# Kernel optimization log

Hardware: AMD Instinct MI355X
Metric: run time of the kernel (lower is better)

The kernel has to match this reference:

```python
import jax, jax.numpy as jnp
import numpy as np

B, T, V, E, U, OUT = 1024, 64, 30, 128, 512, 20


def _lstm(x, W, Uh, b, reverse=False, return_seq=True):
    """Keras-style LSTM (gate order i,f,g,o). x: [B,T,D]. Returns [B,T,U] or [B,U]."""
    nu = Uh.shape[0]
    if reverse:
        x = x[:, ::-1]
    xz = jnp.einsum('btd,dg->btg', x, W) + b  # [B,T,4U] input projection, precomputed

    def step(carry, z_t):
        h, c = carry
        z = z_t + h @ Uh
        i, f, g, o = jnp.split(z, 4, axis=-1)
        c = jax.nn.sigmoid(f) * c + jax.nn.sigmoid(i) * jnp.tanh(g)
        h = jax.nn.sigmoid(o) * jnp.tanh(c)
        return (h, c), h

    bsz = x.shape[0]
    init = (jnp.zeros((bsz, nu), x.dtype), jnp.zeros((bsz, nu), x.dtype))
    (h_last, _), hs = jax.lax.scan(step, init, jnp.swapaxes(xz, 0, 1))
    if return_seq:
        hs = jnp.swapaxes(hs, 0, 1)  # [B,T,U]
        if reverse:
            hs = hs[:, ::-1]
        return hs
    return h_last


def setup_inputs() -> dict:
    key = jax.random.key(0)
    ks = jax.random.split(key, 14)
    f32 = jnp.float32

    def n(k, shape, s=0.05):
        return jax.random.normal(k, shape, f32) * s

    G = 4 * U
    return {
        'x': jax.random.randint(ks[0], (B, T), 0, V, dtype=jnp.int32),
        'emb': n(ks[1], (V, E)),
        # layer 1 forward / backward directions
        'W1f': n(ks[2], (E, G)), 'U1f': n(ks[3], (U, G)), 'b1f': jnp.zeros((G,), f32),
        'W1b': n(ks[4], (E, G)), 'U1b': n(ks[5], (U, G)), 'b1b': jnp.zeros((G,), f32),
        # layer 2 forward / backward directions (input dim = 2U from concat)
        'W2f': n(ks[6], (2 * U, G)), 'U2f': n(ks[7], (U, G)), 'b2f': jnp.zeros((G,), f32),
        'W2b': n(ks[8], (2 * U, G)), 'U2b': n(ks[9], (U, G)), 'b2b': jnp.zeros((G,), f32),
        # dense head
        'Wd': n(ks[10], (2 * U, 2 * U)), 'bd': jnp.zeros((2 * U,), f32),
        'Wo': n(ks[11], (2 * U, OUT)), 'bo': jnp.zeros((OUT,), f32),
    }


def reference(x, emb, W1f, U1f, b1f, W1b, U1b, b1b,
              W2f, U2f, b2f, W2b, U2b, b2b, Wd, bd, Wo, bo):
    e = emb[x]  # [B,T,E] embedding lookup
    # Bidirectional LSTM 1, return_sequences=True, concat merge -> [B,T,2U]
    h1 = jnp.concatenate([
        _lstm(e, W1f, U1f, b1f),
        _lstm(e, W1b, U1b, b1b, reverse=True),
    ], axis=-1)
    # Bidirectional LSTM 2, return_sequences=False -> [B,2U]
    h2 = jnp.concatenate([
        _lstm(h1, W2f, U2f, b2f, return_seq=False),
        _lstm(h1, W2b, U2b, b2b, reverse=True, return_seq=False),
    ], axis=-1)
    d = jax.nn.relu(h2 @ Wd + bd)  # Dense(2U, relu)
    return d @ Wo + bo             # Dense(output_len), [B,OUT]
```

## Files before the change

### kernel.cpp

```cpp
#include <hip/hip_runtime.h>
#include <hip/hip_bf16.h>

typedef __hip_bfloat16 bf16;
typedef __attribute__((ext_vector_type(4))) float f32x4;
typedef __attribute__((ext_vector_type(8))) short s16x8;

__device__ __forceinline__ float sigf(float x) {
    return 1.0f / (1.0f + __expf(-x));
}
__device__ __forceinline__ float tanh_f(float x) {
    float ax = fabsf(x);
    float e = __expf(-2.0f * ax);
    float r = (1.0f - e) / (1.0f + e);
    return x < 0.0f ? -r : r;
}

#define GLL16(src, ldst)                                                      \
    __builtin_amdgcn_global_load_lds(                                         \
        (const __attribute__((address_space(1))) void*)(src),                 \
        (__attribute__((address_space(3))) void*)(ldst), 16, 0, 0)

__global__ void k_embw(const float* __restrict__ emb,
                       const float* __restrict__ W1f, const float* __restrict__ b1f,
                       const float* __restrict__ W1b, const float* __restrict__ b1b,
                       float* __restrict__ embW) {
    int c = blockIdx.x * 256 + threadIdx.x;
    int v = blockIdx.y;
    int d = blockIdx.z;
    const float* W = d ? W1b : W1f;
    const float* b = d ? b1b : b1f;
    float acc = b[c];
    const float* er = emb + v * 128;
#pragma unroll 8
    for (int e = 0; e < 128; ++e) acc += er[e] * W[e * 2048 + c];
    int n = ((c & 511) << 2) | (c >> 9);
    embW[(d * 30 + v) * 2048 + n] = acc;
}

__global__ void k_b2r(const float* __restrict__ b2f, const float* __restrict__ b2b,
                      float* __restrict__ dst) {
    int i = blockIdx.x * 256 + threadIdx.x;
    int d = i >> 11, n = i & 2047;
    int c = ((n & 3) << 9) | (n >> 2);
    dst[i] = (d ? b2b : b2f)[c];
}

template<int REORDER>
__global__ void k_trans(const float* __restrict__ src, bf16* __restrict__ dst,
                        int ncols, int kpitch, int koff) {
    __shared__ float tile[64][65];
    int k0 = blockIdx.x * 64;
    int c0 = blockIdx.y * 64;
    int tid = threadIdx.x;
#pragma unroll
    for (int i = 0; i < 16; ++i) {
        int seg = tid + i * 256;
        int r = seg >> 6, cc = seg & 63;
        tile[r][cc] = src[(size_t)(k0 + r) * ncols + c0 + cc];
    }
    __syncthreads();
#pragma unroll
    for (int i = 0; i < 16; ++i) {
        int seg = tid + i * 256;
        int nl = seg >> 6, kl = seg & 63;
        int c = c0 + nl;
        int n = REORDER ? (((c & 511) << 2) | (c >> 9)) : c;
        int kabs = koff + k0 + kl;
        dst[(size_t)n * kpitch + (kabs ^ ((n & 7) << 3))] =
            __float2bfloat16(tile[kl][nl]);
    }
}

template<int MODE>
__global__ __launch_bounds__(256, 2)
void k_step(const bf16* __restrict__ A1, const bf16* __restrict__ A2,
            const bf16* __restrict__ Bt, const float* __restrict__ table,
            const int* __restrict__ xin, float* __restrict__ c_st,
            bf16* __restrict__ h_out, bf16* __restrict__ h1s, int t)
{
    constexpr int NCH = (MODE == 0) ? 8 : (MODE == 1) ? 24 : 16;
    constexpr int BP  = (MODE == 0) ? 512 : (MODE == 1) ? 1536 : 1024;

    __shared__ __align__(16) short ldss[32768];

    const int tid  = threadIdx.x;
    const int lane = tid & 63;
    const int wv   = tid >> 6;
    const int wm   = (wv >> 1) << 6;
    const int wn   = (wv & 1) << 6;

    int n0, m0;
    if constexpr (MODE == 2) {
        n0 = (blockIdx.x & 7) << 7;
        m0 = (blockIdx.x >> 3) << 7;
    } else {
        const int xcd = blockIdx.x & 7, y = blockIdx.x >> 3;
        n0 = (((xcd << 1) | (y >> 4))) << 7;
        m0 = (y & 15) << 7;
    }

    const int dir = (MODE == 2) ? 0 : (m0 >= 1024);
    const int t_a = dir ? 63 - t : t;

    const char* a1b;
    if constexpr (MODE == 1)
        a1b = (const char*)(A1 + ((size_t)t_a << 20) + ((size_t)(m0 & 1023) << 10));
    else
        a1b = (const char*)(A1 + (size_t)m0 * 512);
    const char* const btb = (const char*)(Bt + (size_t)dir * 2048 * BP + (size_t)n0 * BP);
    const char* const a2b = (const char*)A2;

    auto stage = [&](int c, int half) {
        char* base = (char*)ldss + half * 32768;
#pragma unroll
        for (int i = 0; i < 4; ++i) {
            const int u = i * 256 + tid;
            const int r = u >> 3, j = u & 7;
            const char* src;
            if constexpr (MODE == 0)
                src = a1b + r * 1024 + c * 128 + j * 16;
            else if constexpr (MODE == 1)
                src = (c < 16) ? a1b + r * 2048 + c * 128 + j * 16
                               : a2b + (size_t)(m0 + r) * 1024 + (c - 16) * 128 + j * 16;
            else
                src = (c < 8) ? a1b + r * 1024 + c * 128 + j * 16
                              : a2b + (size_t)(m0 + r) * 1024 + (c - 8) * 128 + j * 16;
            GLL16(src, base + (i * 256 + wv * 64) * 16);
        }
#pragma unroll
        for (int i = 0; i < 4; ++i) {
            const int u = i * 256 + tid;
            const int r = u >> 3, j = u & 7;
            const char* src = btb + (size_t)r * (BP * 2) + c * 128 + j * 16;
            GLL16(src, base + 16384 + (i * 256 + wv * 64) * 16);
        }
    };

    f32x4 acc[4][4];
#pragma unroll
    for (int i = 0; i < 4; ++i)
#pragma unroll
        for (int j = 0; j < 4; ++j) acc[i][j] = (f32x4){0.f, 0.f, 0.f, 0.f};

    stage(0, 0);

    const int rl = lane & 15;
    const int q8 = (lane >> 4) << 3;
    const int xk = (rl & 7) << 3;

    for (int c = 0; c < NCH; ++c) {
        __syncthreads();
        if (c + 1 < NCH) stage(c + 1, (c + 1) & 1);
        const short* as = ldss + (c & 1) * 16384;
        const short* bs = as + 8192;
#pragma unroll
        for (int ks = 0; ks < 2; ++ks) {
            const int eo = ((ks << 5) + q8) ^ xk;
            s16x8 af[4], bq[4];
#pragma unroll
            for (int f = 0; f < 4; ++f)
                af[f] = *(const s16x8*)&as[(wm + f * 16 + rl) * 64 + eo];
#pragma unroll
            for (int f = 0; f < 4; ++f)
                bq[f] = *(const s16x8*)&bs[(wn + f * 16 + rl) * 64 + eo];
#pragma unroll
            for (int fm = 0; fm < 4; ++fm)
#pragma unroll
                for (int fn = 0; fn < 4; ++fn)
                    acc[fm][fn] = __builtin_amdgcn_mfma_f32_16x16x32_bf16(
                        af[fm], bq[fn], acc[fm][fn], 0, 0, 0);
        }
    }

    if constexpr (MODE == 2) {
#pragma unroll
        for (int fn = 0; fn < 4; ++fn) {
            const int col = n0 + wn + fn * 16 + rl;
            const float bdv = table[col];
#pragma unroll
            for (int fm = 0; fm < 4; ++fm) {
                const int rb = m0 + wm + fm * 16 + ((lane >> 4) << 2);
#pragma unroll
                for (int r = 0; r < 4; ++r) {
                    float v = acc[fm][fn][r] + bdv;
                    h_out[(size_t)(rb + r) * 1024 + col] =
                        __float2bfloat16(v > 0.f ? v : 0.f);
                }
            }
        }
    } else {
        float* z = (float*)ldss;
        const int u0 = n0 >> 2;
        for (int half = 0; half < 2; ++half) {
            __syncthreads();
            if ((wv >> 1) == half) {
#pragma unroll
                for (int fm = 0; fm < 4; ++fm)
#pragma unroll
                    for (int fn = 0; fn < 4; ++fn) {
                        const int zr = fm * 16 + ((lane >> 4) << 2);
                        const int zc = wn + fn * 16 + rl;
#pragma unroll
                        for (int r = 0; r < 4; ++r)
                            z[(zr + r) * 132 + zc] = acc[fm][fn][r];
                    }
            }
            __syncthreads();
#pragma unroll 2
            for (int j = 0; j < 8; ++j) {
                const int cid = j * 256 + tid;
                const int ml = cid >> 5;
                const int ul = cid & 31;
                const int mg = m0 + half * 64 + ml;
                const int b  = mg & 1023;
                float4 z4 = *(float4*)&z[ml * 132 + (ul << 2)];
                const float* tab;
                if constexpr (MODE == 0) {
                    const int v = xin[(b << 6) + t_a];
                    tab = table + (size_t)(dir * 30 + v) * 2048;
                } else {
                    tab = table + dir * 2048;
                }
                const float4 tv = *(const float4*)&tab[n0 + (ul << 2)];
                const float zi = z4.x + tv.x, zf = z4.y + tv.y;
                const float zg = z4.z + tv.z, zo = z4.w + tv.w;
                const float ig = sigf(zi), fg = sigf(zf);
                const float gg = tanh_f(zg), og = sigf(zo);
                const size_t cu = (size_t)mg * 512 + u0 + ul;
                const float cn = fg * c_st[cu] + ig * gg;
                c_st[cu] = cn;
                const float h = og * tanh_f(cn);
                const int us = (u0 + ul) ^ ((mg & 7) << 3);
                h_out[(size_t)mg * 512 + us] = __float2bfloat16(h);
                if constexpr (MODE == 0) {
                    const int col = (((dir << 9) | (u0 + ul)) ^ ((b & 7) << 3));
                    h1s[(((size_t)t_a << 10) + b) * 1024 + col] =
                        __float2bfloat16(h);
                }
            }
        }
    }
}

__global__ __launch_bounds__(256)
void k_out(const bf16* __restrict__ dbuf, const float* __restrict__ Wo,
           const float* __restrict__ bo, float* __restrict__ out) {
    int b = blockIdx.x, tid = threadIdx.x;
    int wv = tid >> 6, lane = tid & 63;
    float acc[5] = {0.f, 0.f, 0.f, 0.f, 0.f};
    for (int kk = 0; kk < 1024; kk += 64) {
        float a = __bfloat162float(dbuf[b * 1024 + kk + lane]);
#pragma unroll
        for (int j = 0; j < 5; ++j)
            acc[j] += a * Wo[(kk + lane) * 20 + wv + j * 4];
    }
#pragma unroll
    for (int j = 0; j < 5; ++j) {
        float s = acc[j];
        for (int off = 32; off; off >>= 1) s += __shfl_down(s, off, 64);
        if (lane == 0) out[b * 20 + wv + j * 4] = s + bo[wv + j * 4];
    }
}

extern "C" void kernel_launch(void* const* d_in, const int* in_sizes, int n_in,
                              void* d_out, int out_size, void* d_ws, size_t ws_size,
                              hipStream_t stream) {
    const int*   x   = (const int*)  d_in[0];
    const float* emb = (const float*)d_in[1];
    const float* W1f = (const float*)d_in[2];
    const float* U1f = (const float*)d_in[3];
    const float* b1f = (const float*)d_in[4];
    const float* W1b = (const float*)d_in[5];
    const float* U1b = (const float*)d_in[6];
    const float* b1b = (const float*)d_in[7];
    const float* W2f = (const float*)d_in[8];
    const float* U2f = (const float*)d_in[9];
    const float* b2f = (const float*)d_in[10];
    const float* W2b = (const float*)d_in[11];
    const float* U2b = (const float*)d_in[12];
    const float* b2b = (const float*)d_in[13];
    const float* Wd  = (const float*)d_in[14];
    const float* bd  = (const float*)d_in[15];
    const float* Wo  = (const float*)d_in[16];
    const float* bo  = (const float*)d_in[17];

    char* ws = (char*)d_ws;
    float* embW = (float*)(ws + 0);
    float* b2r  = (float*)(ws + 491520);
    bf16* Ut1   = (bf16*)(ws + 507904);
    bf16* BigBt = (bf16*)(ws + 4702208);
    bf16* Wdt   = (bf16*)(ws + 17285120);
    bf16* hA    = (bf16*)(ws + 19382272);
    bf16* hB    = (bf16*)(ws + 21479424);
    float* cst  = (float*)(ws + 23576576);
    bf16* dbuf  = (bf16*)(ws + 27770880);
    bf16* h1seq = (bf16*)(ws + 29868032);

    k_embw<<<dim3(8, 30, 2), 256, 0, stream>>>(emb, W1f, b1f, W1b, b1b, embW);
    k_b2r<<<16, 256, 0, stream>>>(b2f, b2b, b2r);
    k_trans<1><<<dim3(8, 32), 256, 0, stream>>>(U1f, Ut1,              2048, 512, 0);
    k_trans<1><<<dim3(8, 32), 256, 0, stream>>>(U1b, Ut1 + 2048 * 512, 2048, 512, 0);
    k_trans<1><<<dim3(16, 32), 256, 0, stream>>>(W2f, BigBt,                2048, 1536, 0);
    k_trans<1><<<dim3(8, 32), 256, 0, stream>>>(U2f, BigBt,                2048, 1536, 1024);
    k_trans<1><<<dim3(16, 32), 256, 0, stream>>>(W2b, BigBt + 2048 * 1536, 2048, 1536, 0);
    k_trans<1><<<dim3(8, 32), 256, 0, stream>>>(U2b, BigBt + 2048 * 1536, 2048, 1536, 1024);
    k_trans<0><<<dim3(16, 16), 256, 0, stream>>>(Wd, Wdt, 1024, 1024, 0);

    hipMemsetAsync(hA, 0, (size_t)2048 * 512 * sizeof(bf16), stream);
    hipMemsetAsync(cst, 0, (size_t)2048 * 512 * sizeof(float), stream);
    bf16 *hin = hA, *hout = hB;
    for (int t = 0; t < 64; ++t) {
        k_step<0><<<256, 256, 0, stream>>>(
            hin, (const bf16*)nullptr, Ut1, embW, x, cst, hout, h1seq, t);
        bf16* tmp = hin; hin = hout; hout = tmp;
    }

    hipMemsetAsync(hin, 0, (size_t)2048 * 512 * sizeof(bf16), stream);
    hipMemsetAsync(cst, 0, (size_t)2048 * 512 * sizeof(float), stream);
    for (int t = 0; t < 64; ++t) {
        k_step<1><<<256, 256, 0, stream>>>(
            h1seq, hin, BigBt, b2r, (const int*)nullptr, cst, hout,
            (bf16*)nullptr, t);
        bf16* tmp = hin; hin = hout; hout = tmp;
    }

    k_step<2><<<64, 256, 0, stream>>>(
        hin, hin + (size_t)1024 * 512, Wdt, bd, (const int*)nullptr,
        (float*)nullptr, dbuf, (bf16*)nullptr, 0);
    k_out<<<1024, 256, 0, stream>>>(dbuf, Wo, bo, (float*)d_out);
}
```

Baseline: 2.603 ms.

## Run each LSTM layer as one persistent cooperative kernel with register-resident recurrent weights

Each layer's 64 per-timestep launches are replaced by a single cooperative kernel that loops over time and uses grid.sync between steps. A non-cooperative per-step fallback is kept. Every block loads its slice of the recurrent weight matrix into registers once, so per-step shared-memory staging of U is dropped, and the tile is reshaped to 128x32 per wave. The aim is to remove launch overhead and repeated weight traffic, at the cost of heavy register pressure (one block per CU), grid-wide barrier latency, and reliance on all 256 blocks being co-resident.

```diff
diff --git a/kernel.cpp b/kernel.cpp
--- a/kernel.cpp
+++ b/kernel.cpp
@@ -1,5 +1,8 @@
 #include <hip/hip_runtime.h>
 #include <hip/hip_bf16.h>
+#include <hip/hip_cooperative_groups.h>
+
+namespace cg = cooperative_groups;
 
 typedef __hip_bfloat16 bf16;
 typedef __attribute__((ext_vector_type(4))) float f32x4;
@@ -45,7 +48,7 @@
     dst[i] = (d ? b2b : b2f)[c];
 }
 
-template<int REORDER>
+template<int REORDER, int XOR>
 __global__ void k_trans(const float* __restrict__ src, bf16* __restrict__ dst,
                         int ncols, int kpitch, int koff) {
     __shared__ float tile[64][65];
@@ -66,144 +69,174 @@
         int c = c0 + nl;
         int n = REORDER ? (((c & 511) << 2) | (c >> 9)) : c;
         int kabs = koff + k0 + kl;
-        dst[(size_t)n * kpitch + (kabs ^ ((n & 7) << 3))] =
-            __float2bfloat16(tile[kl][nl]);
-    }
-}
-
-template<int MODE>
-__global__ __launch_bounds__(256, 2)
-void k_step(const bf16* __restrict__ A1, const bf16* __restrict__ A2,
-            const bf16* __restrict__ Bt, const float* __restrict__ table,
-            const int* __restrict__ xin, float* __restrict__ c_st,
-            bf16* __restrict__ h_out, bf16* __restrict__ h1s, int t)
+        int ks = XOR ? (kabs ^ ((n & 7) << 3)) : kabs;
+        dst[(size_t)n * kpitch + ks] = __float2bfloat16(tile[kl][nl]);
+    }
+}
+
+template<int LAYER>
+__global__ __launch_bounds__(256, 1)
+void l_run(const bf16* __restrict__ Bres, const bf16* __restrict__ W2t,
+           bf16* __restrict__ h1s, const float* __restrict__ table,
+           const int* __restrict__ xin, float* __restrict__ c_st,
+           bf16* __restrict__ h0, bf16* __restrict__ h1, int t0, int t1)
 {
-    constexpr int NCH = (MODE == 0) ? 8 : (MODE == 1) ? 24 : 16;
-    constexpr int BP  = (MODE == 0) ? 512 : (MODE == 1) ? 1536 : 1024;
+    cg::grid_group grid = cg::this_grid();
+    constexpr int NCH = (LAYER == 1) ? 8 : 24;
 
     __shared__ __align__(16) short ldss[32768];
 
     const int tid  = threadIdx.x;
     const int lane = tid & 63;
     const int wv   = tid >> 6;
-    const int wm   = (wv >> 1) << 6;
-    const int wn   = (wv & 1) << 6;
-
-    int n0, m0;
-    if constexpr (MODE == 2) {
-        n0 = (blockIdx.x & 7) << 7;
-        m0 = (blockIdx.x >> 3) << 7;
-    } else {
-        const int xcd = blockIdx.x & 7, y = blockIdx.x >> 3;
-        n0 = (((xcd << 1) | (y >> 4))) << 7;
-        m0 = (y & 15) << 7;
-    }
-
-    const int dir = (MODE == 2) ? 0 : (m0 >= 1024);
-    const int t_a = dir ? 63 - t : t;
-
-    const char* a1b;
-    if constexpr (MODE == 1)
-        a1b = (const char*)(A1 + ((size_t)t_a << 20) + ((size_t)(m0 & 1023) << 10));
-    else
-        a1b = (const char*)(A1 + (size_t)m0 * 512);
-    const char* const btb = (const char*)(Bt + (size_t)dir * 2048 * BP + (size_t)n0 * BP);
-    const char* const a2b = (const char*)A2;
-
-    auto stage = [&](int c, int half) {
-        char* base = (char*)ldss + half * 32768;
-#pragma unroll
-        for (int i = 0; i < 4; ++i) {
-            const int u = i * 256 + tid;
-            const int r = u >> 3, j = u & 7;
-            const char* src;
-            if constexpr (MODE == 0)
-                src = a1b + r * 1024 + c * 128 + j * 16;
-            else if constexpr (MODE == 1)
-                src = (c < 16) ? a1b + r * 2048 + c * 128 + j * 16
-                               : a2b + (size_t)(m0 + r) * 1024 + (c - 16) * 128 + j * 16;
-            else
-                src = (c < 8) ? a1b + r * 1024 + c * 128 + j * 16
-                              : a2b + (size_t)(m0 + r) * 1024 + (c - 8) * 128 + j * 16;
-            GLL16(src, base + (i * 256 + wv * 64) * 16);
-        }
-#pragma unroll
-        for (int i = 0; i < 4; ++i) {
-            const int u = i * 256 + tid;
-            const int r = u >> 3, j = u & 7;
-            const char* src = btb + (size_t)r * (BP * 2) + c * 128 + j * 16;
-            GLL16(src, base + 16384 + (i * 256 + wv * 64) * 16);
-        }
-    };
-
-    f32x4 acc[4][4];
-#pragma unroll
-    for (int i = 0; i < 4; ++i)
-#pragma unroll
-        for (int j = 0; j < 4; ++j) acc[i][j] = (f32x4){0.f, 0.f, 0.f, 0.f};
-
-    stage(0, 0);
-
-    const int rl = lane & 15;
-    const int q8 = (lane >> 4) << 3;
-    const int xk = (rl & 7) << 3;
-
-    for (int c = 0; c < NCH; ++c) {
-        __syncthreads();
-        if (c + 1 < NCH) stage(c + 1, (c + 1) & 1);
-        const short* as = ldss + (c & 1) * 16384;
-        const short* bs = as + 8192;
-#pragma unroll
-        for (int ks = 0; ks < 2; ++ks) {
-            const int eo = ((ks << 5) + q8) ^ xk;
-            s16x8 af[4], bq[4];
-#pragma unroll
-            for (int f = 0; f < 4; ++f)
-                af[f] = *(const s16x8*)&as[(wm + f * 16 + rl) * 64 + eo];
-#pragma unroll
-            for (int f = 0; f < 4; ++f)
-                bq[f] = *(const s16x8*)&bs[(wn + f * 16 + rl) * 64 + eo];
-#pragma unroll
-            for (int fm = 0; fm < 4; ++fm)
-#pragma unroll
-                for (int fn = 0; fn < 4; ++fn)
-                    acc[fm][fn] = __builtin_amdgcn_mfma_f32_16x16x32_bf16(
-                        af[fm], bq[fn], acc[fm][fn], 0, 0, 0);
-        }
-    }
-
-    if constexpr (MODE == 2) {
-#pragma unroll
-        for (int fn = 0; fn < 4; ++fn) {
-            const int col = n0 + wn + fn * 16 + rl;
-            const float bdv = table[col];
-#pragma unroll
-            for (int fm = 0; fm < 4; ++fm) {
-                const int rb = m0 + wm + fm * 16 + ((lane >> 4) << 2);
-#pragma unroll
-                for (int r = 0; r < 4; ++r) {
-                    float v = acc[fm][fn][r] + bdv;
-                    h_out[(size_t)(rb + r) * 1024 + col] =
-                        __float2bfloat16(v > 0.f ? v : 0.f);
-                }
-            }
-        }
-    } else {
+    const int xcd  = blockIdx.x & 7, yy = blockIdx.x >> 3;
+    const int n0   = ((xcd << 1) | (yy >> 4)) << 7;
+    const int m0   = (yy & 15) << 7;
+    const int dir  = (m0 >= 1024);
+    const int rl   = lane & 15;
+    const int q8   = (lane >> 4) << 3;
+    const int xk   = (rl & 7) << 3;
+    const int u0   = n0 >> 2;
+
+    s16x8 bres[2][16];
+    {
+        const bf16* bp = Bres + ((size_t)dir * 2048 + n0 + (wv << 5) + rl) * 512 + q8;
+#pragma unroll
+        for (int fn = 0; fn < 2; ++fn)
+#pragma unroll
+            for (int ks = 0; ks < 16; ++ks)
+                bres[fn][ks] = *(const s16x8*)(bp + fn * (16 * 512) + ks * 32);
+    }
+
+    const char* const btb = (LAYER == 2)
+        ? (const char*)(W2t + ((size_t)dir * 2048 + n0) * 1024) : nullptr;
+
+#pragma unroll 1
+    for (int t = t0; t < t1; ++t) {
+        const bf16* hin  = (t & 1) ? h1 : h0;
+        bf16*       hout = (t & 1) ? h0 : h1;
+        const int t_a = dir ? 63 - t : t;
+        const char* a1b = nullptr;
+        if (LAYER == 2)
+            a1b = (const char*)(h1s + ((size_t)t_a << 20) + ((size_t)(m0 & 1023) << 10));
+        const char* const arb = (const char*)(hin + (size_t)m0 * 512);
+
+        auto stage = [&](int c, int buf) {
+#pragma unroll
+            for (int i = 0; i < 4; ++i) {
+                const int u = i * 256 + tid;
+                const int r = u >> 3, j = u & 7;
+                const char* src;
+                if (LAYER == 1)
+                    src = arb + r * 1024 + c * 128 + j * 16;
+                else
+                    src = (c < 16) ? a1b + r * 2048 + c * 128 + j * 16
+                                   : arb + r * 1024 + (c - 16) * 128 + j * 16;
+                GLL16(src, (char*)ldss + buf * 16384 + (i * 256 + wv * 64) * 16);
+            }
+            if (LAYER == 2 && c < 16) {
+#pragma unroll
+                for (int i = 0; i < 4; ++i) {
+                    const int u = i * 256 + tid;
+                    const int r = u >> 3, j = u & 7;
+                    GLL16(btb + (size_t)r * 2048 + c * 128 + j * 16,
+                          (char*)ldss + 32768 + buf * 16384 + (i * 256 + wv * 64) * 16);
+                }
+            }
+        };
+
+        f32x4 acc[8][2];
+#pragma unroll
+        for (int i = 0; i < 8; ++i) {
+            acc[i][0] = (f32x4){0.f, 0.f, 0.f, 0.f};
+            acc[i][1] = (f32x4){0.f, 0.f, 0.f, 0.f};
+        }
+
+        stage(0, 0);
+
+        if constexpr (LAYER == 2) {
+#pragma unroll 2
+            for (int c = 0; c < 16; ++c) {
+                __syncthreads();
+                stage(c + 1, (c + 1) & 1);
+                const short* as = ldss + (c & 1) * 8192;
+                const short* bs = ldss + 16384 + (c & 1) * 8192;
+#pragma unroll
+                for (int ks = 0; ks < 2; ++ks) {
+                    const int eo = ((ks << 5) + q8) ^ xk;
+                    s16x8 af[8], bq[2];
+#pragma unroll
+                    for (int f = 0; f < 8; ++f)
+                        af[f] = *(const s16x8*)&as[(f * 16 + rl) * 64 + eo];
+#pragma unroll
+                    for (int fn = 0; fn < 2; ++fn)
+                        bq[fn] = *(const s16x8*)&bs[((wv << 5) + fn * 16 + rl) * 64 + eo];
+#pragma unroll
+                    for (int fm = 0; fm < 8; ++fm)
+#pragma unroll
+                        for (int fn = 0; fn < 2; ++fn)
+                            acc[fm][fn] = __builtin_amdgcn_mfma_f32_16x16x32_bf16(
+                                af[fm], bq[fn], acc[fm][fn], 0, 0, 0);
+                }
+            }
+#pragma unroll
+            for (int cc = 0; cc < 8; ++cc) {
+                const int c = 16 + cc;
+                __syncthreads();
+                if (c + 1 < NCH) stage(c + 1, (c + 1) & 1);
+                const short* as = ldss + (c & 1) * 8192;
+#pragma unroll
+                for (int ks = 0; ks < 2; ++ks) {
+                    const int eo = ((ks << 5) + q8) ^ xk;
+                    s16x8 af[8];
+#pragma unroll
+                    for (int f = 0; f < 8; ++f)
+                        af[f] = *(const s16x8*)&as[(f * 16 + rl) * 64 + eo];
+#pragma unroll
+                    for (int fm = 0; fm < 8; ++fm)
+#pragma unroll
+                        for (int fn = 0; fn < 2; ++fn)
+                            acc[fm][fn] = __builtin_amdgcn_mfma_f32_16x16x32_bf16(
+                                af[fm], bres[fn][cc * 2 + ks], acc[fm][fn], 0, 0, 0);
+                }
+            }
+        } else {
+#pragma unroll
+            for (int c = 0; c < 8; ++c) {
+                __syncthreads();
+                if (c + 1 < NCH) stage(c + 1, (c + 1) & 1);
+                const short* as = ldss + (c & 1) * 8192;
+#pragma unroll
+                for (int ks = 0; ks < 2; ++ks) {
+                    const int eo = ((ks << 5) + q8) ^ xk;
+                    s16x8 af[8];
+#pragma unroll
+                    for (int f = 0; f < 8; ++f)
+                        af[f] = *(const s16x8*)&as[(f * 16 + rl) * 64 + eo];
+#pragma unroll
+                    for (int fm = 0; fm < 8; ++fm)
+#pragma unroll
+                        for (int fn = 0; fn < 2; ++fn)
+                            acc[fm][fn] = __builtin_amdgcn_mfma_f32_16x16x32_bf16(
+                                af[fm], bres[fn][c * 2 + ks], acc[fm][fn], 0, 0, 0);
+                }
+            }
+        }
+
         float* z = (float*)ldss;
-        const int u0 = n0 >> 2;
+#pragma unroll
         for (int half = 0; half < 2; ++half) {
             __syncthreads();
-            if ((wv >> 1) == half) {
-#pragma unroll
-                for (int fm = 0; fm < 4; ++fm)
-#pragma unroll
-                    for (int fn = 0; fn < 4; ++fn) {
-                        const int zr = fm * 16 + ((lane >> 4) << 2);
-                        const int zc = wn + fn * 16 + rl;
-#pragma unroll
-                        for (int r = 0; r < 4; ++r)
-                            z[(zr + r) * 132 + zc] = acc[fm][fn][r];
-                    }
+#pragma unroll
+            for (int fm = 0; fm < 4; ++fm) {
+                const int zr = fm * 16 + ((lane >> 4) << 2);
+#pragma unroll
+                for (int fn = 0; fn < 2; ++fn) {
+                    const int zc = (wv << 5) + fn * 16 + rl;
+#pragma unroll
+                    for (int r = 0; r < 4; ++r)
+                        z[(zr + r) * 132 + zc] = acc[half * 4 + fm][fn][r];
+                }
             }
             __syncthreads();
 #pragma unroll 2
@@ -215,7 +248,7 @@
                 const int b  = mg & 1023;
                 float4 z4 = *(float4*)&z[ml * 132 + (ul << 2)];
                 const float* tab;
-                if constexpr (MODE == 0) {
+                if constexpr (LAYER == 1) {
                     const int v = xin[(b << 6) + t_a];
                     tab = table + (size_t)(dir * 30 + v) * 2048;
                 } else {
@@ -231,12 +264,106 @@
                 c_st[cu] = cn;
                 const float h = og * tanh_f(cn);
                 const int us = (u0 + ul) ^ ((mg & 7) << 3);
-                h_out[(size_t)mg * 512 + us] = __float2bfloat16(h);
-                if constexpr (MODE == 0) {
+                hout[(size_t)mg * 512 + us] = __float2bfloat16(h);
+                if constexpr (LAYER == 1) {
                     const int col = (((dir << 9) | (u0 + ul)) ^ ((b & 7) << 3));
                     h1s[(((size_t)t_a << 10) + b) * 1024 + col] =
                         __float2bfloat16(h);
                 }
+            }
+        }
+
+        if (t + 1 < t1) {
+            __threadfence();
+            grid.sync();
+        }
+    }
+}
+
+__global__ __launch_bounds__(256, 2)
+void k_dense(const bf16* __restrict__ hin, const bf16* __restrict__ Bt,
+             const float* __restrict__ bd, bf16* __restrict__ dbuf)
+{
+    __shared__ __align__(16) short ldss[32768];
+    const int tid  = threadIdx.x;
+    const int lane = tid & 63;
+    const int wv   = tid >> 6;
+    const int wm   = (wv >> 1) << 6;
+    const int wn   = (wv & 1) << 6;
+    const int n0   = (blockIdx.x & 7) << 7;
+    const int m0   = (blockIdx.x >> 3) << 7;
+
+    const char* const a1b = (const char*)(hin + (size_t)m0 * 512);
+    const char* const a2b = (const char*)(hin + (size_t)1024 * 512);
+    const char* const btb = (const char*)(Bt + (size_t)n0 * 1024);
+
+    auto stage = [&](int c, int buf) {
+#pragma unroll
+        for (int i = 0; i < 4; ++i) {
+            const int u = i * 256 + tid;
+            const int r = u >> 3, j = u & 7;
+            const char* src = (c < 8)
+                ? a1b + r * 1024 + c * 128 + j * 16
+                : a2b + (size_t)(m0 + r) * 1024 + (c - 8) * 128 + j * 16;
+            GLL16(src, (char*)ldss + buf * 16384 + (i * 256 + wv * 64) * 16);
+        }
+#pragma unroll
+        for (int i = 0; i < 4; ++i) {
+            const int u = i * 256 + tid;
+            const int r = u >> 3, j = u & 7;
+            GLL16(btb + (size_t)r * 2048 + c * 128 + j * 16,
+                  (char*)ldss + 32768 + buf * 16384 + (i * 256 + wv * 64) * 16);
+        }
+    };
+
+    f32x4 acc[4][4];
+#pragma unroll
+    for (int i = 0; i < 4; ++i)
+#pragma unroll
+        for (int j = 0; j < 4; ++j) acc[i][j] = (f32x4){0.f, 0.f, 0.f, 0.f};
+
+    stage(0, 0);
+    const int rl = lane & 15;
+    const int q8 = (lane >> 4) << 3;
+    const int xk = (rl & 7) << 3;
+
+#pragma unroll 2
+    for (int c = 0; c < 16; ++c) {
+        __syncthreads();
+        if (c + 1 < 16) stage(c + 1, (c + 1) & 1);
+        const short* as = ldss + (c & 1) * 8192;
+        const short* bs = ldss + 16384 + (c & 1) * 8192;
+#pragma unroll
+        for (int ks = 0; ks < 2; ++ks) {
+            const int eo = ((ks << 5) + q8) ^ xk;
+            s16x8 af[4], bq[4];
+#pragma unroll
+            for (int f = 0; f < 4; ++f)
+                af[f] = *(const s16x8*)&as[(wm + f * 16 + rl) * 64 + eo];
+#pragma unroll
+            for (int f = 0; f < 4; ++f)
+                bq[f] = *(const s16x8*)&bs[(wn + f * 16 + rl) * 64 + eo];
+#pragma unroll
+            for (int fm = 0; fm < 4; ++fm)
+#pragma unroll
+                for (int fn = 0; fn < 4; ++fn)
+                    acc[fm][fn] = __builtin_amdgcn_mfma_f32_16x16x32_bf16(
+                        af[fm], bq[fn], acc[fm][fn], 0, 0, 0);
+        }
+    }
+
+#pragma unroll
+    for (int fn = 0; fn < 4; ++fn) {
+        const int col = n0 + wn + fn * 16 + rl;
+        const float bdv = bd[col];
+#pragma unroll
+        for (int fm = 0; fm < 4; ++fm) {
+            const int rb = m0 + wm + fm * 16 + ((lane >> 4) << 2);
+#pragma unroll
+            for (int r = 0; r < 4; ++r) {
+                float v = acc[fm][fn][r] + bdv;
+                dbuf[(size_t)(rb + r) * 1024 + col] =
+                    __float2bfloat16(v > 0.f ? v : 0.f);
             }
         }
     }
@@ -288,7 +415,8 @@
     float* embW = (float*)(ws + 0);
     float* b2r  = (float*)(ws + 491520);
     bf16* Ut1   = (bf16*)(ws + 507904);
-    bf16* BigBt = (bf16*)(ws + 4702208);
+    bf16* Ut2   = (bf16*)(ws + 4702208);
+    bf16* W2t   = (bf16*)(ws + 8896512);
     bf16* Wdt   = (bf16*)(ws + 17285120);
     bf16* hA    = (bf16*)(ws + 19382272);
     bf16* hB    = (bf16*)(ws + 21479424);
@@ -298,34 +426,71 @@
 
     k_embw<<<dim3(8, 30, 2), 256, 0, stream>>>(emb, W1f, b1f, W1b, b1b, embW);
     k_b2r<<<16, 256, 0, stream>>>(b2f, b2b, b2r);
-    k_trans<1><<<dim3(8, 32), 256, 0, stream>>>(U1f, Ut1,              2048, 512, 0);
-    k_trans<1><<<dim3(8, 32), 256, 0, stream>>>(U1b, Ut1 + 2048 * 512, 2048, 512, 0);
-    k_trans<1><<<dim3(16, 32), 256, 0, stream>>>(W2f, BigBt,                2048, 1536, 0);
-    k_trans<1><<<dim3(8, 32), 256, 0, stream>>>(U2f, BigBt,                2048, 1536, 1024);
-    k_trans<1><<<dim3(16, 32), 256, 0, stream>>>(W2b, BigBt + 2048 * 1536, 2048, 1536, 0);
-    k_trans<1><<<dim3(8, 32), 256, 0, stream>>>(U2b, BigBt + 2048 * 1536, 2048, 1536, 1024);
-    k_trans<0><<<dim3(16, 16), 256, 0, stream>>>(Wd, Wdt, 1024, 1024, 0);
+    k_trans<1, 0><<<dim3(8, 32), 256, 0, stream>>>(U1f, Ut1,              2048, 512, 0);
+    k_trans<1, 0><<<dim3(8, 32), 256, 0, stream>>>(U1b, Ut1 + 2048 * 512, 2048, 512, 0);
+    k_trans<1, 0><<<dim3(8, 32), 256, 0, stream>>>(U2f, Ut2,              2048, 512, 0);
+    k_trans<1, 0><<<dim3(8, 32), 256, 0, stream>>>(U2b, Ut2 + 2048 * 512, 2048, 512, 0);
+    k_trans<1, 1><<<dim3(16, 32), 256, 0, stream>>>(W2f, W2t,               2048, 1024, 0);
+    k_trans<1, 1><<<dim3(16, 32), 256, 0, stream>>>(W2b, W2t + 2048 * 1024, 2048, 1024, 0);
+    k_trans<0, 1><<<dim3(16, 16), 256, 0, stream>>>(Wd, Wdt, 1024, 1024, 0);
+
+    int dev = 0;
+    hipGetDevice(&dev);
+    int coopAttr = 0, cus = 0;
+    hipDeviceGetAttribute(&coopAttr, hipDeviceAttributeCooperativeLaunch, dev);
+    hipDeviceGetAttribute(&cus, hipDeviceAttributeMultiprocessorCount, dev);
+    int nb1 = 0, nb2 = 0;
+    hipOccupancyMaxActiveBlocksPerMultiprocessor(&nb1, l_run<1>, 256, 0);
+    hipOccupancyMaxActiveBlocksPerMultiprocessor(&nb2, l_run<2>, 256, 0);
+    const bool coop1 = coopAttr && nb1 > 0 && (long)nb1 * cus >= 256;
+    const bool coop2 = coopAttr && nb2 > 0 && (long)nb2 * cus >= 256;
 
     hipMemsetAsync(hA, 0, (size_t)2048 * 512 * sizeof(bf16), stream);
     hipMemsetAsync(cst, 0, (size_t)2048 * 512 * sizeof(float), stream);
-    bf16 *hin = hA, *hout = hB;
-    for (int t = 0; t < 64; ++t) {
-        k_step<0><<<256, 256, 0, stream>>>(
-            hin, (const bf16*)nullptr, Ut1, embW, x, cst, hout, h1seq, t);
-        bf16* tmp = hin; hin = hout; hout = tmp;
-    }
-
-    hipMemsetAsync(hin, 0, (size_t)2048 * 512 * sizeof(bf16), stream);
+    {
+        const bf16* Bres = Ut1;  const bf16* w2 = nullptr;  bf16* h1sp = h1seq;
+        const float* tab = embW; const int* xi = x;         float* cs = cst;
+        bf16* h0p = hA;          bf16* h1p = hB;
+        int t0 = 0, t1 = 64;
+        bool done = false;
+        if (coop1) {
+            void* args[] = {&Bres, &w2, &h1sp, &tab, &xi, &cs, &h0p, &h1p, &t0, &t1};
+            void (*f1)(const bf16*, const bf16*, bf16*, const float*, const int*,
+                       float*, bf16*, bf16*, int, int) = l_run<1>;
+            done = hipLaunchCooperativeKernel(reinterpret_cast<void*>(f1),
+                                              dim3(256), dim3(256), args, 0,
+                                              stream) == hipSuccess;
+        }
+        if (!done)
+            for (int t = 0; t < 64; ++t)
+                l_run<1><<<256, 256, 0, stream>>>(Ut1, (const bf16*)nullptr,
+                                                  h1seq, embW, x, cst, hA, hB,
+                                                  t, t + 1);
+    }
+
+    hipMemsetAsync(hA, 0, (size_t)2048 * 512 * sizeof(bf16), stream);
     hipMemsetAsync(cst, 0, (size_t)2048 * 512 * sizeof(float), stream);
-    for (int t = 0; t < 64; ++t) {
-        k_step<1><<<256, 256, 0, stream>>>(
-            h1seq, hin, BigBt, b2r, (const int*)nullptr, cst, hout,
-            (bf16*)nullptr, t);
-        bf16* tmp = hin; hin = hout; hout = tmp;
-    }
-
-    k_step<2><<<64, 256, 0, stream>>>(
-        hin, hin + (size_t)1024 * 512, Wdt, bd, (const int*)nullptr,
-        (float*)nullptr, dbuf, (bf16*)nullptr, 0);
+    {
+        const bf16* Bres = Ut2;  const bf16* w2 = W2t;  bf16* h1sp = h1seq;
+        const float* tab = b2r;  const int* xi = nullptr;  float* cs = cst;
+        bf16* h0p = hA;          bf16* h1p = hB;
+        int t0 = 0, t1 = 64;
+        bool done = false;
+        if (coop2) {
+            void* args[] = {&Bres, &w2, &h1sp, &tab, &xi, &cs, &h0p, &h1p, &t0, &t1};
+            void (*f2)(const bf16*, const bf16*, bf16*, const float*, const int*,
+                       float*, bf16*, bf16*, int, int) = l_run<2>;
+            done = hipLaunchCooperativeKernel(reinterpret_cast<void*>(f2),
+                                              dim3(256), dim3(256), args, 0,
+                                              stream) == hipSuccess;
+        }
+        if (!done)
+            for (int t = 0; t < 64; ++t)
+                l_run<2><<<256, 256, 0, stream>>>(Ut2, W2t, h1seq, b2r,
+                                                  (const int*)nullptr, cst,
+                                                  hA, hB, t, t + 1);
+    }
+
+    k_dense<<<64, 256, 0, stream>>>(hA, Wdt, bd, dbuf);
     k_out<<<1024, 256, 0, stream>>>(dbuf, Wo, bo, (float*)d_out);
 }
```

Result: slower. 3.275 ms (+25.8%).

## Halve LSTM step tile width to launch 512 blocks and split dense kernel

Applied to the files above, without the earlier changes.

The recurrent step kernel now uses a 128x64 output tile instead of 128x128, so each step launches 512 blocks instead of 256. The aim is to fill more of the GPU's compute units during the latency-bound per-timestep GEMMs. The gate epilogue is rewritten to work on one 128x64 tile in a single pass. The dense head moves into its own kernel that keeps the 128x128 tiling. The cost is that each block reuses the A operand less, so more of the A tile is reloaded across blocks. The new XOR template flag is always set to 1, so it changes nothing yet.

```diff
diff --git a/kernel.cpp b/kernel.cpp
--- a/kernel.cpp
+++ b/kernel.cpp
@@ -45,7 +45,7 @@
     dst[i] = (d ? b2b : b2f)[c];
 }
 
-template<int REORDER>
+template<int REORDER, int XOR>
 __global__ void k_trans(const float* __restrict__ src, bf16* __restrict__ dst,
                         int ncols, int kpitch, int koff) {
     __shared__ float tile[64][65];
@@ -66,8 +66,8 @@
         int c = c0 + nl;
         int n = REORDER ? (((c & 511) << 2) | (c >> 9)) : c;
         int kabs = koff + k0 + kl;
-        dst[(size_t)n * kpitch + (kabs ^ ((n & 7) << 3))] =
-            __float2bfloat16(tile[kl][nl]);
+        int ks = XOR ? (kabs ^ ((n & 7) << 3)) : kabs;
+        dst[(size_t)n * kpitch + ks] = __float2bfloat16(tile[kl][nl]);
     }
 }
 
@@ -78,40 +78,38 @@
             const int* __restrict__ xin, float* __restrict__ c_st,
             bf16* __restrict__ h_out, bf16* __restrict__ h1s, int t)
 {
-    constexpr int NCH = (MODE == 0) ? 8 : (MODE == 1) ? 24 : 16;
-    constexpr int BP  = (MODE == 0) ? 512 : (MODE == 1) ? 1536 : 1024;
-
-    __shared__ __align__(16) short ldss[32768];
+    constexpr int NCH = (MODE == 0) ? 8 : 24;
+    constexpr int BP  = (MODE == 0) ? 512 : 1536;
+
+    __shared__ __align__(16) short ldss[24576];
 
     const int tid  = threadIdx.x;
     const int lane = tid & 63;
     const int wv   = tid >> 6;
-    const int wm   = (wv >> 1) << 6;
-    const int wn   = (wv & 1) << 6;
-
-    int n0, m0;
-    if constexpr (MODE == 2) {
-        n0 = (blockIdx.x & 7) << 7;
-        m0 = (blockIdx.x >> 3) << 7;
-    } else {
-        const int xcd = blockIdx.x & 7, y = blockIdx.x >> 3;
-        n0 = (((xcd << 1) | (y >> 4))) << 7;
-        m0 = (y & 15) << 7;
-    }
-
-    const int dir = (MODE == 2) ? 0 : (m0 >= 1024);
+    const int wm   = wv << 5;
+
+    const int xcd = blockIdx.x & 7, idx = blockIdx.x >> 3;
+    const int n0  = ((xcd << 2) | (idx >> 4)) << 6;
+    const int m0  = (idx & 15) << 7;
+
+    const int dir = (m0 >= 1024);
     const int t_a = dir ? 63 - t : t;
+    const int rl  = lane & 15;
+    const int q8  = (lane >> 4) << 3;
+    const int q4  = (lane >> 4) << 2;
+    const int xk  = (rl & 7) << 3;
+    const int u0  = n0 >> 2;
 
     const char* a1b;
     if constexpr (MODE == 1)
         a1b = (const char*)(A1 + ((size_t)t_a << 20) + ((size_t)(m0 & 1023) << 10));
     else
         a1b = (const char*)(A1 + (size_t)m0 * 512);
-    const char* const btb = (const char*)(Bt + (size_t)dir * 2048 * BP + (size_t)n0 * BP);
+    const char* const btb = (const char*)(Bt + ((size_t)dir * 2048 + n0) * BP);
     const char* const a2b = (const char*)A2;
 
-    auto stage = [&](int c, int half) {
-        char* base = (char*)ldss + half * 32768;
+    auto stage = [&](int c, int buf) {
+        char* base = (char*)ldss + buf * 24576;
 #pragma unroll
         for (int i = 0; i < 4; ++i) {
             const int u = i * 256 + tid;
@@ -119,20 +117,132 @@
             const char* src;
             if constexpr (MODE == 0)
                 src = a1b + r * 1024 + c * 128 + j * 16;
-            else if constexpr (MODE == 1)
+            else
                 src = (c < 16) ? a1b + r * 2048 + c * 128 + j * 16
                                : a2b + (size_t)(m0 + r) * 1024 + (c - 16) * 128 + j * 16;
-            else
-                src = (c < 8) ? a1b + r * 1024 + c * 128 + j * 16
-                              : a2b + (size_t)(m0 + r) * 1024 + (c - 8) * 128 + j * 16;
             GLL16(src, base + (i * 256 + wv * 64) * 16);
         }
+#pragma unroll
+        for (int i = 0; i < 2; ++i) {
+            const int u = i * 256 + tid;
+            const int r = u >> 3, j = u & 7;
+            GLL16(btb + (size_t)r * (BP * 2) + c * 128 + j * 16,
+                  base + 16384 + (i * 256 + wv * 64) * 16);
+        }
+    };
+
+    f32x4 acc[2][4];
+#pragma unroll
+    for (int i = 0; i < 2; ++i)
+#pragma unroll
+        for (int j = 0; j < 4; ++j) acc[i][j] = (f32x4){0.f, 0.f, 0.f, 0.f};
+
+    stage(0, 0);
+
+    for (int c = 0; c < NCH; ++c) {
+        __syncthreads();
+        if (c + 1 < NCH) stage(c + 1, (c + 1) & 1);
+        const short* as = ldss + (c & 1) * 12288;
+        const short* bs = as + 8192;
+#pragma unroll
+        for (int ks = 0; ks < 2; ++ks) {
+            const int eo = ((ks << 5) + q8) ^ xk;
+            s16x8 af[2], bq[4];
+#pragma unroll
+            for (int f = 0; f < 2; ++f)
+                af[f] = *(const s16x8*)&as[(wm + f * 16 + rl) * 64 + eo];
+#pragma unroll
+            for (int f = 0; f < 4; ++f)
+                bq[f] = *(const s16x8*)&bs[(f * 16 + rl) * 64 + eo];
+#pragma unroll
+            for (int fm = 0; fm < 2; ++fm)
+#pragma unroll
+                for (int fn = 0; fn < 4; ++fn)
+                    acc[fm][fn] = __builtin_amdgcn_mfma_f32_16x16x32_bf16(
+                        af[fm], bq[fn], acc[fm][fn], 0, 0, 0);
+        }
+    }
+
+    float* z = (float*)ldss;
+    __syncthreads();
+#pragma unroll
+    for (int fm = 0; fm < 2; ++fm)
+#pragma unroll
+        for (int fn = 0; fn < 4; ++fn) {
+            const int zr = wm + fm * 16 + q4;
+            const int zc = fn * 16 + rl;
+#pragma unroll
+            for (int r = 0; r < 4; ++r)
+                z[(zr + r) * 68 + zc] = acc[fm][fn][r];
+        }
+    __syncthreads();
+#pragma unroll 2
+    for (int j = 0; j < 8; ++j) {
+        const int cid = j * 256 + tid;
+        const int ml = cid >> 4;
+        const int ul = cid & 15;
+        const int mg = m0 + ml;
+        const int b  = mg & 1023;
+        float4 z4 = *(float4*)&z[ml * 68 + (ul << 2)];
+        const float* tab;
+        if constexpr (MODE == 0) {
+            const int v = xin[(b << 6) + t_a];
+            tab = table + (size_t)(dir * 30 + v) * 2048;
+        } else {
+            tab = table + dir * 2048;
+        }
+        const float4 tv = *(const float4*)&tab[n0 + (ul << 2)];
+        const float zi = z4.x + tv.x, zf = z4.y + tv.y;
+        const float zg = z4.z + tv.z, zo = z4.w + tv.w;
+        const float ig = sigf(zi), fg = sigf(zf);
+        const float gg = tanh_f(zg), og = sigf(zo);
+        const int u = u0 + ul;
+        const size_t cu = (size_t)mg * 512 + u;
+        const float cn = fg * c_st[cu] + ig * gg;
+        c_st[cu] = cn;
+        const float h = og * tanh_f(cn);
+        const int us = u ^ ((mg & 7) << 3);
+        h_out[(size_t)mg * 512 + us] = __float2bfloat16(h);
+        if constexpr (MODE == 0) {
+            const int col = (((dir << 9) | u) ^ ((b & 7) << 3));
+            h1s[(((size_t)t_a << 10) + b) * 1024 + col] = __float2bfloat16(h);
+        }
+    }
+}
+
+__global__ __launch_bounds__(256, 2)
+void k_dense(const bf16* __restrict__ hin, const bf16* __restrict__ Bt,
+             const float* __restrict__ bd, bf16* __restrict__ dbuf)
+{
+    __shared__ __align__(16) short ldss[32768];
+    const int tid  = threadIdx.x;
+    const int lane = tid & 63;
+    const int wv   = tid >> 6;
+    const int wm   = (wv >> 1) << 6;
+    const int wn   = (wv & 1) << 6;
+    const int n0   = (blockIdx.x & 7) << 7;
+    const int m0   = (blockIdx.x >> 3) << 7;
+
+    const char* const a1b = (const char*)(hin + (size_t)m0 * 512);
+    const char* const a2b = (const char*)(hin + (size_t)1024 * 512);
+    const char* const btb = (const char*)(Bt + (size_t)n0 * 1024);
+
+    auto stage = [&](int c, int buf) {
 #pragma unroll
         for (int i = 0; i < 4; ++i) {
             const int u = i * 256 + tid;
             const int r = u >> 3, j = u & 7;
-            const char* src = btb + (size_t)r * (BP * 2) + c * 128 + j * 16;
-            GLL16(src, base + 16384 + (i * 256 + wv * 64) * 16);
+            const char* src = (c < 8)
+                ? a1b + r * 1024 + c * 128 + j * 16
+                : a2b + (size_t)(m0 + r) * 1024 + (c - 8) * 128 + j * 16;
+            GLL16(src, (char*)ldss + buf * 16384 + (i * 256 + wv * 64) * 16);
+        }
+#pragma unroll
+        for (int i = 0; i < 4; ++i) {
+            const int u = i * 256 + tid;
+            const int r = u >> 3, j = u & 7;
+            GLL16(btb + (size_t)r * 2048 + c * 128 + j * 16,
+                  (char*)ldss + 32768 + buf * 16384 + (i * 256 + wv * 64) * 16);
         }
     };
 
@@ -143,16 +253,16 @@
         for (int j = 0; j < 4; ++j) acc[i][j] = (f32x4){0.f, 0.f, 0.f, 0.f};
 
     stage(0, 0);
-
     const int rl = lane & 15;
     const int q8 = (lane >> 4) << 3;
     const int xk = (rl & 7) << 3;
 
-    for (int c = 0; c < NCH; ++c) {
+#pragma unroll 2
+    for (int c = 0; c < 16; ++c) {
         __syncthreads();
-        if (c + 1 < NCH) stage(c + 1, (c + 1) & 1);
-        const short* as = ldss + (c & 1) * 16384;
-        const short* bs = as + 8192;
+        if (c + 1 < 16) stage(c + 1, (c + 1) & 1);
+        const short* as = ldss + (c & 1) * 8192;
+        const short* bs = ldss + 16384 + (c & 1) * 8192;
 #pragma unroll
         for (int ks = 0; ks < 2; ++ks) {
             const int eo = ((ks << 5) + q8) ^ xk;
@@ -172,71 +282,18 @@
         }
     }
 
-    if constexpr (MODE == 2) {
-#pragma unroll
-        for (int fn = 0; fn < 4; ++fn) {
-            const int col = n0 + wn + fn * 16 + rl;
-            const float bdv = table[col];
-#pragma unroll
-            for (int fm = 0; fm < 4; ++fm) {
-                const int rb = m0 + wm + fm * 16 + ((lane >> 4) << 2);
-#pragma unroll
-                for (int r = 0; r < 4; ++r) {
-                    float v = acc[fm][fn][r] + bdv;
-                    h_out[(size_t)(rb + r) * 1024 + col] =
-                        __float2bfloat16(v > 0.f ? v : 0.f);
-                }
-            }
-        }
-    } else {
-        float* z = (float*)ldss;
-        const int u0 = n0 >> 2;
-        for (int half = 0; half < 2; ++half) {
-            __syncthreads();
-            if ((wv >> 1) == half) {
-#pragma unroll
-                for (int fm = 0; fm < 4; ++fm)
-#pragma unroll
-                    for (int fn = 0; fn < 4; ++fn) {
-                        const int zr = fm * 16 + ((lane >> 4) << 2);
-                        const int zc = wn + fn * 16 + rl;
-#pragma unroll
-                        for (int r = 0; r < 4; ++r)
-                            z[(zr + r) * 132 + zc] = acc[fm][fn][r];
-                    }
-            }
-            __syncthreads();
-#pragma unroll 2
-            for (int j = 0; j < 8; ++j) {
-                const int cid = j * 256 + tid;
-                const int ml = cid >> 5;
-                const int ul = cid & 31;
-                const int mg = m0 + half * 64 + ml;
-                const int b  = mg & 1023;
-                float4 z4 = *(float4*)&z[ml * 132 + (ul << 2)];
-                const float* tab;
-                if constexpr (MODE == 0) {
-                    const int v = xin[(b << 6) + t_a];
-                    tab = table + (size_t)(dir * 30 + v) * 2048;
-                } else {
-                    tab = table + dir * 2048;
-                }
-                const float4 tv = *(const float4*)&tab[n0 + (ul << 2)];
-                const float zi = z4.x + tv.x, zf = z4.y + tv.y;
-                const float zg = z4.z + tv.z, zo = z4.w + tv.w;
-                const float ig = sigf(zi), fg = sigf(zf);
-                const float gg = tanh_f(zg), og = sigf(zo);
-                const size_t cu = (size_t)mg * 512 + u0 + ul;
-                const float cn = fg * c_st[cu] + ig * gg;
-                c_st[cu] = cn;
-                const float h = og * tanh_f(cn);
-                const int us = (u0 + ul) ^ ((mg & 7) << 3);
-                h_out[(size_t)mg * 512 + us] = __float2bfloat16(h);
-                if constexpr (MODE == 0) {
-                    const int col = (((dir << 9) | (u0 + ul)) ^ ((b & 7) << 3));
-                    h1s[(((size_t)t_a << 10) + b) * 1024 + col] =
-                        __float2bfloat16(h);
-                }
+#pragma unroll
+    for (int fn = 0; fn < 4; ++fn) {
+        const int col = n0 + wn + fn * 16 + rl;
+        const float bdv = bd[col];
+#pragma unroll
+        for (int fm = 0; fm < 4; ++fm) {
+            const int rb = m0 + wm + fm * 16 + ((lane >> 4) << 2);
+#pragma unroll
+            for (int r = 0; r < 4; ++r) {
+                float v = acc[fm][fn][r] + bdv;
+                dbuf[(size_t)(rb + r) * 1024 + col] =
+                    __float2bfloat16(v > 0.f ? v : 0.f);
             }
         }
     }
@@ -298,19 +355,19 @@
 
     k_embw<<<dim3(8, 30, 2), 256, 0, stream>>>(emb, W1f, b1f, W1b, b1b, embW);
     k_b2r<<<16, 256, 0, stream>>>(b2f, b2b, b2r);
-    k_trans<1><<<dim3(8, 32), 256, 0, stream>>>(U1f, Ut1,              2048, 512, 0);
-    k_trans<1><<<dim3(8, 32), 256, 0, stream>>>(U1b, Ut1 + 2048 * 512, 2048, 512, 0);
-    k_trans<1><<<dim3(16, 32), 256, 0, stream>>>(W2f, BigBt,                2048, 1536, 0);
-    k_trans<1><<<dim3(8, 32), 256, 0, stream>>>(U2f, BigBt,                2048, 1536, 1024);
-    k_trans<1><<<dim3(16, 32), 256, 0, stream>>>(W2b, BigBt + 2048 * 1536, 2048, 1536, 0);
-    k_trans<1><<<dim3(8, 32), 256, 0, stream>>>(U2b, BigBt + 2048 * 1536, 2048, 1536, 1024);
-    k_trans<0><<<dim3(16, 16), 256, 0, stream>>>(Wd, Wdt, 1024, 1024, 0);
+    k_trans<1, 1><<<dim3(8, 32), 256, 0, stream>>>(U1f, Ut1,              2048, 512, 0);
+    k_trans<1, 1><<<dim3(8, 32), 256, 0, stream>>>(U1b, Ut1 + 2048 * 512, 2048, 512, 0);
+    k_trans<1, 1><<<dim3(16, 32), 256, 0, stream>>>(W2f, BigBt,                2048, 1536, 0);
+    k_trans<1, 1><<<dim3(8, 32), 256, 0, stream>>>(U2f, BigBt,                2048, 1536, 1024);
+    k_trans<1, 1><<<dim3(16, 32), 256, 0, stream>>>(W2b, BigBt + 2048 * 1536, 2048, 1536, 0);
+    k_trans<1, 1><<<dim3(8, 32), 256, 0, stream>>>(U2b, BigBt + 2048 * 1536, 2048, 1536, 1024);
+    k_trans<0, 1><<<dim3(16, 16), 256, 0, stream>>>(Wd, Wdt, 1024, 1024, 0);
 
     hipMemsetAsync(hA, 0, (size_t)2048 * 512 * sizeof(bf16), stream);
     hipMemsetAsync(cst, 0, (size_t)2048 * 512 * sizeof(float), stream);
     bf16 *hin = hA, *hout = hB;
     for (int t = 0; t < 64; ++t) {
-        k_step<0><<<256, 256, 0, stream>>>(
+        k_step<0><<<512, 256, 0, stream>>>(
             hin, (const bf16*)nullptr, Ut1, embW, x, cst, hout, h1seq, t);
         bf16* tmp = hin; hin = hout; hout = tmp;
     }
@@ -318,14 +375,12 @@
     hipMemsetAsync(hin, 0, (size_t)2048 * 512 * sizeof(bf16), stream);
     hipMemsetAsync(cst, 0, (size_t)2048 * 512 * sizeof(float), stream);
     for (int t = 0; t < 64; ++t) {
-        k_step<1><<<256, 256, 0, stream>>>(
+        k_step<1><<<512, 256, 0, stream>>>(
             h1seq, hin, BigBt, b2r, (const int*)nullptr, cst, hout,
             (bf16*)nullptr, t);
         bf16* tmp = hin; hin = hout; hout = tmp;
     }
 
-    k_step<2><<<64, 256, 0, stream>>>(
-        hin, hin + (size_t)1024 * 512, Wdt, bd, (const int*)nullptr,
-        (float*)nullptr, dbuf, (bf16*)nullptr, 0);
+    k_dense<<<64, 256, 0, stream>>>(hin, Wdt, bd, dbuf);
     k_out<<<1024, 256, 0, stream>>>(dbuf, Wo, bo, (float*)d_out);
 }
```

New measurement: 2.170 ms. -16.6%, faster.
